# Kernel tuning notes

Measured on AMD Instinct MI355X. Metric: run time of the kernel, lower is better.

## Reference

```python
import jax, jax.numpy as jnp
import numpy as np

EPS = 1e-8  # torch nn.CosineSimilarity default eps

def setup_inputs() -> dict:
    key = jax.random.key(0)
    kx, ky = jax.random.split(key)
    x = jax.random.normal(kx, (8, 2048, 512), dtype=jnp.float32)
    y = jax.random.normal(ky, (8, 2048, 512), dtype=jnp.float32)
    return {"x": x, "y": y}

def reference(x, y):
    # cosine(x_i, y_j) = <x_i, y_j> / max(||x_i|| * ||y_j||, eps)
    # GEMM form instead of the O(n^2 d) broadcast-expand.
    dots = jnp.einsum('bnd,bmd->bnm', x, y)            # [bs, n, n]
    xn = jnp.linalg.norm(x, axis=-1)                   # [bs, n]
    yn = jnp.linalg.norm(y, axis=-1)                   # [bs, n]
    denom = jnp.maximum(xn[:, :, None] * yn[:, None, :], EPS)
    return dots / denom
```

## Files before the change

### kernel.cpp

```cpp
#include <hip/hip_runtime.h>

#define BATCH 8
#define NROW  2048
#define DIM   512

typedef __bf16 bf16x8 __attribute__((ext_vector_type(8)));
typedef float  f32x4  __attribute__((ext_vector_type(4)));

typedef __attribute__((address_space(3))) void       lds_t;
typedef const __attribute__((address_space(1))) void gmem_t;

__device__ __forceinline__ unsigned short f2bf(float f) {
    unsigned int u = __float_as_uint(f);
    u += 0x7FFFu + ((u >> 16) & 1u);
    return (unsigned short)(u >> 16);
}

__global__ __launch_bounds__(256) void prep_kernel(
    const float* __restrict__ x, const float* __restrict__ y,
    unsigned short* __restrict__ xbf, unsigned short* __restrict__ ybf,
    float* __restrict__ rxn, float* __restrict__ ryn)
{
    const int wave = threadIdx.x >> 6;
    const int lane = threadIdx.x & 63;
    const int row  = blockIdx.x * 4 + wave;

    const float* src; unsigned short* dst; float* rn;
    if (blockIdx.y == 0) { src = x; dst = xbf; rn = rxn; }
    else                 { src = y; dst = ybf; rn = ryn; }

    const float4* s4 = (const float4*)(src + (size_t)row * DIM);
    ushort4*      d4 = (ushort4*)(dst + (size_t)row * DIM);

    float ss = 0.f;
#pragma unroll
    for (int h = 0; h < 2; ++h) {
        float4 v = s4[h * 64 + lane];
        ss += v.x * v.x + v.y * v.y + v.z * v.z + v.w * v.w;
        ushort4 o;
        o.x = f2bf(v.x); o.y = f2bf(v.y); o.z = f2bf(v.z); o.w = f2bf(v.w);
        d4[h * 64 + lane] = o;
    }
#pragma unroll
    for (int off = 32; off; off >>= 1) ss += __shfl_xor(ss, off, 64);
    if (lane == 0) rn[row] = 1.0f / sqrtf(ss);
}


#define STAGE(Xp, Xi, K, T)                                                  \
  { char* hb_ = sm + (((((T) & 1) << 2) | ((Xi) << 1) | (K)) << 14);         \
    __builtin_amdgcn_global_load_lds(                                        \
      (gmem_t*)((Xp) + (size_t)vr0 * DIM + (T) * 64 + (K) * 32 + vc),        \
      (lds_t*)(hb_ + wave * 1024), 16, 0, 0);                                \
    __builtin_amdgcn_global_load_lds(                                        \
      (gmem_t*)((Xp) + (size_t)vr1 * DIM + (T) * 64 + (K) * 32 + vc),        \
      (lds_t*)(hb_ + 8192 + wave * 1024), 16, 0, 0); }

#define LDSA(M, KS, PAR) \
  (*(const bf16x8*)(sm + ((((PAR) << 2) | (KS)) << 14) + ((wm * 8 + (M)) << 10) + rb))
#define LDSB(N, KS, PAR) \
  (*(const bf16x8*)(sm + ((((PAR) << 2) | 2 | (KS)) << 14) + ((wn * 4 + (N)) << 10) + rb))

#define PHASE(PAR, MH, KS, READB, STAGE_STMT, VM_STMT)                       \
  { __builtin_amdgcn_sched_barrier(0);                                       \
    bf16x8 a0 = LDSA((MH)*4+0, KS, PAR), a1 = LDSA((MH)*4+1, KS, PAR),       \
           a2 = LDSA((MH)*4+2, KS, PAR), a3 = LDSA((MH)*4+3, KS, PAR);       \
    if (READB) { bfr[0] = LDSB(0, KS, PAR); bfr[1] = LDSB(1, KS, PAR);       \
                 bfr[2] = LDSB(2, KS, PAR); bfr[3] = LDSB(3, KS, PAR); }     \
    STAGE_STMT;                                                              \
    __builtin_amdgcn_s_barrier();                                            \
    asm volatile("s_waitcnt lgkmcnt(0)" ::: "memory");                       \
    VM_STMT;                                                                 \
    __builtin_amdgcn_sched_barrier(0);                                       \
    __builtin_amdgcn_s_setprio(1);                                           \
    _Pragma("unroll")                                                        \
    for (int n = 0; n < 4; ++n) {                                            \
      acc[(MH)*4+0][n] = __builtin_amdgcn_mfma_f32_16x16x32_bf16(a0, bfr[n], acc[(MH)*4+0][n], 0, 0, 0); \
      acc[(MH)*4+1][n] = __builtin_amdgcn_mfma_f32_16x16x32_bf16(a1, bfr[n], acc[(MH)*4+1][n], 0, 0, 0); \
      acc[(MH)*4+2][n] = __builtin_amdgcn_mfma_f32_16x16x32_bf16(a2, bfr[n], acc[(MH)*4+2][n], 0, 0, 0); \
      acc[(MH)*4+3][n] = __builtin_amdgcn_mfma_f32_16x16x32_bf16(a3, bfr[n], acc[(MH)*4+3][n], 0, 0, 0); \
    }                                                                        \
    __builtin_amdgcn_s_setprio(0);                                           \
    __builtin_amdgcn_sched_barrier(0);                                       \
    __builtin_amdgcn_s_barrier(); }

#define VM6 asm volatile("s_waitcnt vmcnt(6)" ::: "memory")
#define VM0 asm volatile("s_waitcnt vmcnt(0)" ::: "memory")

__global__ __launch_bounds__(512) void gemm_kernel(
    const __bf16* __restrict__ xbf, const __bf16* __restrict__ ybf,
    const float* __restrict__ rxn, const float* __restrict__ ryn,
    float* __restrict__ out)
{
    extern __shared__ char sm[];
    const int tid  = threadIdx.x;
    const int lane = tid & 63;
    const int wave = tid >> 6;
    const int wm   = wave >> 2;
    const int wn   = wave & 3;

    const int bid = blockIdx.x;
    const int wg  = (bid & 7) * 64 + (bid >> 3);
    const int b   = wg >> 6;
    const int bm  = (wg >> 3) & 7;
    const int bn  = wg & 7;

    const __bf16* Ap = xbf + ((size_t)b * NROW + bm * 256) * DIM;
    const __bf16* Bp = ybf + ((size_t)b * NROW + bn * 256) * DIM;

    const int vr0 = wave * 16 + (lane >> 2);
    const int vr1 = vr0 + 128;
    const int vc  = ((lane & 3) * 8) ^ ((lane & 32) ? 16 : 0);
    const int rb  = (lane & 15) * 64 + (((lane >> 4) * 16) ^ ((lane & 8) ? 32 : 0));

    STAGE(Bp, 1, 0, 0) STAGE(Ap, 0, 0, 0) STAGE(Bp, 1, 1, 0) STAGE(Ap, 0, 1, 0)
    STAGE(Bp, 1, 0, 1) STAGE(Ap, 0, 0, 1) STAGE(Bp, 1, 1, 1)
    VM6;
    __builtin_amdgcn_sched_barrier(0);
    __builtin_amdgcn_s_barrier();

    f32x4 acc[8][4] = {};
    bf16x8 bfr[4];

    for (int i = 0; i < 4; ++i) {
        const int t1 = 2 * i + 1, t2 = 2 * i + 2, t3 = 2 * i + 3;
        const bool full = (i < 3);
        PHASE(0, 0, 0, 1, STAGE(Ap, 0, 1, t1), )
        PHASE(0, 1, 0, 0, if (full) STAGE(Bp, 1, 0, t2), )
        PHASE(0, 0, 1, 1, if (full) STAGE(Ap, 0, 0, t2), )
        PHASE(0, 1, 1, 0, if (full) STAGE(Bp, 1, 1, t2), if (full) { VM6; } else { VM0; })
        PHASE(1, 0, 0, 1, if (full) STAGE(Ap, 0, 1, t2), )
        PHASE(1, 1, 0, 0, if (full) STAGE(Bp, 1, 0, t3), )
        PHASE(1, 0, 1, 1, if (full) STAGE(Ap, 0, 0, t3), )
        PHASE(1, 1, 1, 0, if (full) STAGE(Bp, 1, 1, t3), if (full) { VM6; })
    }

    const int col = lane & 15;
    const int r4  = (lane >> 4) * 4;
    const int gm0 = bm * 256 + wm * 128;
    const int gn0 = bn * 256 + wn * 64;
    float* C = out + (size_t)b * NROW * NROW;
    const float* rxb = rxn + b * NROW;
    const float* ryb = ryn + b * NROW;

    float ryv[4];
#pragma unroll
    for (int n = 0; n < 4; ++n) ryv[n] = ryb[gn0 + n * 16 + col];

#pragma unroll
    for (int m = 0; m < 8; ++m) {
#pragma unroll
        for (int j = 0; j < 4; ++j) {
            const int gm = gm0 + m * 16 + r4 + j;
            const float rx = rxb[gm];
            float* Crow = C + (size_t)gm * NROW + gn0;
#pragma unroll
            for (int n = 0; n < 4; ++n)
                Crow[n * 16 + col] = acc[m][n][j] * rx * ryv[n];
        }
    }
}

extern "C" void kernel_launch(void* const* d_in, const int* in_sizes, int n_in,
                              void* d_out, int out_size, void* d_ws, size_t ws_size,
                              hipStream_t stream)
{
    const float* x = (const float*)d_in[0];
    const float* y = (const float*)d_in[1];
    float* out = (float*)d_out;

    char* ws = (char*)d_ws;
    unsigned short* xbf = (unsigned short*)ws;
    unsigned short* ybf = (unsigned short*)(ws + ((size_t)16 << 20));
    float* rxn = (float*)(ws + ((size_t)32 << 20));
    float* ryn = rxn + BATCH * NROW;

    static bool attr_done = false;
    if (!attr_done) {
        hipFuncSetAttribute((const void*)gemm_kernel,
                            hipFuncAttributeMaxDynamicSharedMemorySize, 131072);
        attr_done = true;
    }

    prep_kernel<<<dim3(4096, 2), 256, 0, stream>>>(x, y, xbf, ybf, rxn, ryn);
    gemm_kernel<<<dim3(512), 512, 131072, stream>>>(
        (const __bf16*)xbf, (const __bf16*)ybf, rxn, ryn, out);
}
```

Measured before the change: 215.6 us.

## Fuse bf16 conversion and norm computation into the GEMM main loop

Removes the separate prep kernel. The GEMM now loads fp32 tiles of x and y into registers, converts them to bf16, writes them to LDS itself and accumulates row sums of squares on the way. Norms are reduced per block and passed through LDS for the epilogue. This avoids the extra launch and the bf16 round trip through global memory. In exchange the async global-to-LDS loads become register-staged loads with a deeper software pipeline, and each block re-reads and re-converts fp32 input that other blocks also load.

```diff
diff --git a/kernel.cpp b/kernel.cpp
--- a/kernel.cpp
+++ b/kernel.cpp
@@ -6,9 +6,7 @@
 
 typedef __bf16 bf16x8 __attribute__((ext_vector_type(8)));
 typedef float  f32x4  __attribute__((ext_vector_type(4)));
-
-typedef __attribute__((address_space(3))) void       lds_t;
-typedef const __attribute__((address_space(1))) void gmem_t;
+typedef unsigned short u16x8 __attribute__((ext_vector_type(8)));
 
 __device__ __forceinline__ unsigned short f2bf(float f) {
     unsigned int u = __float_as_uint(f);
@@ -16,62 +14,48 @@
     return (unsigned short)(u >> 16);
 }
 
-__global__ __launch_bounds__(256) void prep_kernel(
-    const float* __restrict__ x, const float* __restrict__ y,
-    unsigned short* __restrict__ xbf, unsigned short* __restrict__ ybf,
-    float* __restrict__ rxn, float* __restrict__ ryn)
-{
-    const int wave = threadIdx.x >> 6;
-    const int lane = threadIdx.x & 63;
-    const int row  = blockIdx.x * 4 + wave;
-
-    const float* src; unsigned short* dst; float* rn;
-    if (blockIdx.y == 0) { src = x; dst = xbf; rn = rxn; }
-    else                 { src = y; dst = ybf; rn = ryn; }
-
-    const float4* s4 = (const float4*)(src + (size_t)row * DIM);
-    ushort4*      d4 = (ushort4*)(dst + (size_t)row * DIM);
-
-    float ss = 0.f;
-#pragma unroll
-    for (int h = 0; h < 2; ++h) {
-        float4 v = s4[h * 64 + lane];
-        ss += v.x * v.x + v.y * v.y + v.z * v.z + v.w * v.w;
-        ushort4 o;
-        o.x = f2bf(v.x); o.y = f2bf(v.y); o.z = f2bf(v.z); o.w = f2bf(v.w);
-        d4[h * 64 + lane] = o;
-    }
-#pragma unroll
-    for (int off = 32; off; off >>= 1) ss += __shfl_xor(ss, off, 64);
-    if (lane == 0) rn[row] = 1.0f / sqrtf(ss);
-}
-
-
-#define STAGE(Xp, Xi, K, T)                                                  \
-  { char* hb_ = sm + (((((T) & 1) << 2) | ((Xi) << 1) | (K)) << 14);         \
-    __builtin_amdgcn_global_load_lds(                                        \
-      (gmem_t*)((Xp) + (size_t)vr0 * DIM + (T) * 64 + (K) * 32 + vc),        \
-      (lds_t*)(hb_ + wave * 1024), 16, 0, 0);                                \
-    __builtin_amdgcn_global_load_lds(                                        \
-      (gmem_t*)((Xp) + (size_t)vr1 * DIM + (T) * 64 + (K) * 32 + vc),        \
-      (lds_t*)(hb_ + 8192 + wave * 1024), 16, 0, 0); }
+
+#define LOADH(Xf, K, T, S) {                                                 \
+    const float* p_ = (Xf) + (size_t)vr0 * DIM + (T) * 64 + (K) * 32 + vc;   \
+    st[S][0] = *(const f32x4*)p_;                                            \
+    st[S][1] = *(const f32x4*)(p_ + 4);                                      \
+    const float* q_ = p_ + (size_t)128 * DIM;                                \
+    st[S][2] = *(const f32x4*)q_;                                            \
+    st[S][3] = *(const f32x4*)(q_ + 4);                                      \
+  }
+
+#define WRITEH(Xi, K, T, S, SSa, SSb) {                                      \
+    char* hb_ = sm + (((((T) & 1) << 2) | ((Xi) << 1) | (K)) << 14);         \
+    u16x8 w0_, w1_;                                                          \
+    _Pragma("unroll")                                                        \
+    for (int j_ = 0; j_ < 4; ++j_) {                                         \
+      float v0_ = st[S][0][j_], v1_ = st[S][1][j_];                          \
+      float v2_ = st[S][2][j_], v3_ = st[S][3][j_];                          \
+      SSa += v0_ * v0_ + v1_ * v1_;                                          \
+      SSb += v2_ * v2_ + v3_ * v3_;                                          \
+      w0_[j_] = f2bf(v0_); w0_[j_ + 4] = f2bf(v1_);                          \
+      w1_[j_] = f2bf(v2_); w1_[j_ + 4] = f2bf(v3_);                          \
+    }                                                                        \
+    *(u16x8*)(hb_ + wave * 1024 + lane * 16) = w0_;                          \
+    *(u16x8*)(hb_ + 8192 + wave * 1024 + lane * 16) = w1_;                   \
+  }
 
 #define LDSA(M, KS, PAR) \
   (*(const bf16x8*)(sm + ((((PAR) << 2) | (KS)) << 14) + ((wm * 8 + (M)) << 10) + rb))
 #define LDSB(N, KS, PAR) \
   (*(const bf16x8*)(sm + ((((PAR) << 2) | 2 | (KS)) << 14) + ((wn * 4 + (N)) << 10) + rb))
 
-#define PHASE(PAR, MH, KS, READB, STAGE_STMT, VM_STMT)                       \
+#define PHASE(PAR, MH, KS, READB, LSTMT, WSTMT)                              \
   { __builtin_amdgcn_sched_barrier(0);                                       \
     bf16x8 a0 = LDSA((MH)*4+0, KS, PAR), a1 = LDSA((MH)*4+1, KS, PAR),       \
            a2 = LDSA((MH)*4+2, KS, PAR), a3 = LDSA((MH)*4+3, KS, PAR);       \
     if (READB) { bfr[0] = LDSB(0, KS, PAR); bfr[1] = LDSB(1, KS, PAR);       \
                  bfr[2] = LDSB(2, KS, PAR); bfr[3] = LDSB(3, KS, PAR); }     \
-    STAGE_STMT;                                                              \
+    LSTMT;                                                                   \
+    WSTMT;                                                                   \
+    asm volatile("s_waitcnt lgkmcnt(0)" ::: "memory");                       \
+    __builtin_amdgcn_sched_barrier(0);                                       \
     __builtin_amdgcn_s_barrier();                                            \
-    asm volatile("s_waitcnt lgkmcnt(0)" ::: "memory");                       \
-    VM_STMT;                                                                 \
-    __builtin_amdgcn_sched_barrier(0);                                       \
     __builtin_amdgcn_s_setprio(1);                                           \
     _Pragma("unroll")                                                        \
     for (int n = 0; n < 4; ++n) {                                            \
@@ -84,12 +68,8 @@
     __builtin_amdgcn_sched_barrier(0);                                       \
     __builtin_amdgcn_s_barrier(); }
 
-#define VM6 asm volatile("s_waitcnt vmcnt(6)" ::: "memory")
-#define VM0 asm volatile("s_waitcnt vmcnt(0)" ::: "memory")
-
-__global__ __launch_bounds__(512) void gemm_kernel(
-    const __bf16* __restrict__ xbf, const __bf16* __restrict__ ybf,
-    const float* __restrict__ rxn, const float* __restrict__ ryn,
+__global__ __launch_bounds__(512, 2) void fused_kernel(
+    const float* __restrict__ x, const float* __restrict__ y,
     float* __restrict__ out)
 {
     extern __shared__ char sm[];
@@ -105,55 +85,99 @@
     const int bm  = (wg >> 3) & 7;
     const int bn  = wg & 7;
 
-    const __bf16* Ap = xbf + ((size_t)b * NROW + bm * 256) * DIM;
-    const __bf16* Bp = ybf + ((size_t)b * NROW + bn * 256) * DIM;
+    const float* Af = x + ((size_t)b * NROW + bm * 256) * DIM;
+    const float* Bf = y + ((size_t)b * NROW + bn * 256) * DIM;
 
     const int vr0 = wave * 16 + (lane >> 2);
-    const int vr1 = vr0 + 128;
     const int vc  = ((lane & 3) * 8) ^ ((lane & 32) ? 16 : 0);
     const int rb  = (lane & 15) * 64 + (((lane >> 4) * 16) ^ ((lane & 8) ? 32 : 0));
 
-    STAGE(Bp, 1, 0, 0) STAGE(Ap, 0, 0, 0) STAGE(Bp, 1, 1, 0) STAGE(Ap, 0, 1, 0)
-    STAGE(Bp, 1, 0, 1) STAGE(Ap, 0, 0, 1) STAGE(Bp, 1, 1, 1)
-    VM6;
+    f32x4 st[3][4];
+    float ssA0 = 0.f, ssA1 = 0.f, ssB0 = 0.f, ssB1 = 0.f;
+    f32x4 acc_init;
+    (void)acc_init;
+    f32x4 acc[8][4] = {};
+    bf16x8 bfr[4];
+
+    LOADH(Bf, 0, 0, 0) LOADH(Af, 0, 0, 1)
+    WRITEH(1, 0, 0, 0, ssB0, ssB1) WRITEH(0, 0, 0, 1, ssA0, ssA1)
+    LOADH(Bf, 1, 0, 0) LOADH(Af, 1, 0, 1)
+    WRITEH(1, 1, 0, 0, ssB0, ssB1) WRITEH(0, 1, 0, 1, ssA0, ssA1)
+    LOADH(Bf, 0, 1, 0) LOADH(Af, 0, 1, 1) LOADH(Bf, 1, 1, 2)
+    WRITEH(1, 1, 1, 2, ssB0, ssB1)
+    asm volatile("s_waitcnt lgkmcnt(0)" ::: "memory");
     __builtin_amdgcn_sched_barrier(0);
     __builtin_amdgcn_s_barrier();
 
-    f32x4 acc[8][4] = {};
-    bf16x8 bfr[4];
-
-    for (int i = 0; i < 4; ++i) {
-        const int t1 = 2 * i + 1, t2 = 2 * i + 2, t3 = 2 * i + 3;
-        const bool full = (i < 3);
-        PHASE(0, 0, 0, 1, STAGE(Ap, 0, 1, t1), )
-        PHASE(0, 1, 0, 0, if (full) STAGE(Bp, 1, 0, t2), )
-        PHASE(0, 0, 1, 1, if (full) STAGE(Ap, 0, 0, t2), )
-        PHASE(0, 1, 1, 0, if (full) STAGE(Bp, 1, 1, t2), if (full) { VM6; } else { VM0; })
-        PHASE(1, 0, 0, 1, if (full) STAGE(Ap, 0, 1, t2), )
-        PHASE(1, 1, 0, 0, if (full) STAGE(Bp, 1, 0, t3), )
-        PHASE(1, 0, 1, 1, if (full) STAGE(Ap, 0, 0, t3), )
-        PHASE(1, 1, 1, 0, if (full) STAGE(Bp, 1, 1, t3), if (full) { VM6; })
+    PHASE(0,0,0,1, LOADH(Af,1,1,2), WRITEH(1,0,1, 0, ssB0,ssB1))
+    PHASE(0,1,0,0, LOADH(Bf,0,2,0), WRITEH(0,0,1, 1, ssA0,ssA1))
+    PHASE(0,0,1,1, LOADH(Af,0,2,1), WRITEH(0,1,1, 2, ssA0,ssA1))
+    PHASE(0,1,1,0, LOADH(Bf,1,2,2), WRITEH(1,0,2, 0, ssB0,ssB1))
+    PHASE(1,0,0,1, LOADH(Af,1,2,0), WRITEH(0,0,2, 1, ssA0,ssA1))
+    PHASE(1,1,0,0, LOADH(Bf,0,3,1), WRITEH(1,1,2, 2, ssB0,ssB1))
+    PHASE(1,0,1,1, LOADH(Af,0,3,2), WRITEH(0,1,2, 0, ssA0,ssA1))
+    PHASE(1,1,1,0, LOADH(Bf,1,3,0), WRITEH(1,0,3, 1, ssB0,ssB1))
+    PHASE(0,0,0,1, LOADH(Af,1,3,1), WRITEH(0,0,3, 2, ssA0,ssA1))
+    PHASE(0,1,0,0, LOADH(Bf,0,4,2), WRITEH(1,1,3, 0, ssB0,ssB1))
+    PHASE(0,0,1,1, LOADH(Af,0,4,0), WRITEH(0,1,3, 1, ssA0,ssA1))
+    PHASE(0,1,1,0, LOADH(Bf,1,4,1), WRITEH(1,0,4, 2, ssB0,ssB1))
+    PHASE(1,0,0,1, LOADH(Af,1,4,2), WRITEH(0,0,4, 0, ssA0,ssA1))
+    PHASE(1,1,0,0, LOADH(Bf,0,5,0), WRITEH(1,1,4, 1, ssB0,ssB1))
+    PHASE(1,0,1,1, LOADH(Af,0,5,1), WRITEH(0,1,4, 2, ssA0,ssA1))
+    PHASE(1,1,1,0, LOADH(Bf,1,5,2), WRITEH(1,0,5, 0, ssB0,ssB1))
+    PHASE(0,0,0,1, LOADH(Af,1,5,0), WRITEH(0,0,5, 1, ssA0,ssA1))
+    PHASE(0,1,0,0, LOADH(Bf,0,6,1), WRITEH(1,1,5, 2, ssB0,ssB1))
+    PHASE(0,0,1,1, LOADH(Af,0,6,2), WRITEH(0,1,5, 0, ssA0,ssA1))
+    PHASE(0,1,1,0, LOADH(Bf,1,6,0), WRITEH(1,0,6, 1, ssB0,ssB1))
+    PHASE(1,0,0,1, LOADH(Af,1,6,1), WRITEH(0,0,6, 2, ssA0,ssA1))
+    PHASE(1,1,0,0, LOADH(Bf,0,7,2), WRITEH(1,1,6, 0, ssB0,ssB1))
+    PHASE(1,0,1,1, LOADH(Af,0,7,0), WRITEH(0,1,6, 1, ssA0,ssA1))
+    PHASE(1,1,1,0, LOADH(Bf,1,7,1), WRITEH(1,0,7, 2, ssB0,ssB1))
+    PHASE(0,0,0,1, LOADH(Af,1,7,2), WRITEH(0,0,7, 0, ssA0,ssA1))
+    PHASE(0,1,0,0, ,                WRITEH(1,1,7, 1, ssB0,ssB1))
+    PHASE(0,0,1,1, ,                WRITEH(0,1,7, 2, ssA0,ssA1))
+    PHASE(0,1,1,0, , )
+    PHASE(1,0,0,1, , )
+    PHASE(1,1,0,0, , )
+    PHASE(1,0,1,1, , )
+    PHASE(1,1,1,0, , )
+
+    ssA0 += __shfl_xor(ssA0, 1); ssA0 += __shfl_xor(ssA0, 2);
+    ssA1 += __shfl_xor(ssA1, 1); ssA1 += __shfl_xor(ssA1, 2);
+    ssB0 += __shfl_xor(ssB0, 1); ssB0 += __shfl_xor(ssB0, 2);
+    ssB1 += __shfl_xor(ssB1, 1); ssB1 += __shfl_xor(ssB1, 2);
+
+    float* rxs = (float*)sm;
+    float* rys = rxs + 256;
+    __syncthreads();
+    if ((lane & 3) == 0) {
+        const int r = wave * 16 + (lane >> 2);
+        rxs[r]       = 1.0f / sqrtf(ssA0);
+        rxs[r + 128] = 1.0f / sqrtf(ssA1);
+        rys[r]       = 1.0f / sqrtf(ssB0);
+        rys[r + 128] = 1.0f / sqrtf(ssB1);
     }
+    __syncthreads();
 
     const int col = lane & 15;
     const int r4  = (lane >> 4) * 4;
-    const int gm0 = bm * 256 + wm * 128;
-    const int gn0 = bn * 256 + wn * 64;
+    const int lm0 = wm * 128;
+    const int ln0 = wn * 64;
+    const int gm0 = bm * 256 + lm0;
+    const int gn0 = bn * 256 + ln0;
     float* C = out + (size_t)b * NROW * NROW;
-    const float* rxb = rxn + b * NROW;
-    const float* ryb = ryn + b * NROW;
 
     float ryv[4];
 #pragma unroll
-    for (int n = 0; n < 4; ++n) ryv[n] = ryb[gn0 + n * 16 + col];
+    for (int n = 0; n < 4; ++n) ryv[n] = rys[ln0 + n * 16 + col];
 
 #pragma unroll
     for (int m = 0; m < 8; ++m) {
 #pragma unroll
         for (int j = 0; j < 4; ++j) {
-            const int gm = gm0 + m * 16 + r4 + j;
-            const float rx = rxb[gm];
-            float* Crow = C + (size_t)gm * NROW + gn0;
+            const int lr = lm0 + m * 16 + r4 + j;
+            const float rx = rxs[lr];
+            float* Crow = C + (size_t)(gm0 + m * 16 + r4 + j) * NROW + gn0;
 #pragma unroll
             for (int n = 0; n < 4; ++n)
                 Crow[n * 16 + col] = acc[m][n][j] * rx * ryv[n];
@@ -169,20 +193,12 @@
     const float* y = (const float*)d_in[1];
     float* out = (float*)d_out;
 
-    char* ws = (char*)d_ws;
-    unsigned short* xbf = (unsigned short*)ws;
-    unsigned short* ybf = (unsigned short*)(ws + ((size_t)16 << 20));
-    float* rxn = (float*)(ws + ((size_t)32 << 20));
-    float* ryn = rxn + BATCH * NROW;
-
     static bool attr_done = false;
     if (!attr_done) {
-        hipFuncSetAttribute((const void*)gemm_kernel,
+        hipFuncSetAttribute((const void*)fused_kernel,
                             hipFuncAttributeMaxDynamicSharedMemorySize, 131072);
         attr_done = true;
     }
 
-    prep_kernel<<<dim3(4096, 2), 256, 0, stream>>>(x, y, xbf, ybf, rxn, ryn);
-    gemm_kernel<<<dim3(512), 512, 131072, stream>>>(
-        (const __bf16*)xbf, (const __bf16*)ybf, rxn, ryn, out);
+    fused_kernel<<<dim3(512), 512, 131072, stream>>>(x, y, out);
 }
```

After: 260.5 us. 20.8% more time.
